# Optimization experiments

Hardware: AMD Instinct MI355X
Metric: run time of the kernel (lower is better)

Reference implementation:

```python
import jax, jax.numpy as jnp
import numpy as np

B, T = 64, 2048
HID, FAST, SLOW, VOCAB = 256, 64, 256, 64
WRITE_THRESH = 0.4
NEG = -1000000000.0


def setup_inputs() -> dict:
    key = jax.random.key(0)
    ks = jax.random.split(key, 10)
    s = 0.05  # small init so gate sigmoids are not saturated
    return {
        "seq": jax.random.randint(ks[0], (B, T), 0, VOCAB),
        "emb": jax.random.normal(ks[1], (VOCAB, HID), jnp.float32),        # encoder embedding table
        "Wg": jax.random.normal(ks[2], (HID, 1), jnp.float32) * s,         # write_gate
        "bg": jnp.zeros((1,), jnp.float32),
        "Wd": jax.random.normal(ks[3], (HID, 1), jnp.float32) * s,         # demotion_net
        "bd": jnp.zeros((1,), jnp.float32),
        "Wq": jax.random.normal(ks[4], (HID, HID), jnp.float32) * s,       # read_head.q_proj
        "bq": jnp.zeros((HID,), jnp.float32),
        "Wo": jax.random.normal(ks[5], (HID, VOCAB), jnp.float32) * s,     # read_head.out
        "bo": jnp.zeros((VOCAB,), jnp.float32),
    }


def _process_sequence(h, Wg, bg, Wd, bd):
    # h: (B, T, H). Sequential LRU tiered-memory scatter, vectorized over batch.
    Bb, Tt, H = h.shape

    def step(state, tok_h):
        fm, sm, fa, sa, fu, su = state
        ws = jax.nn.sigmoid(tok_h @ Wg + bg)[:, 0]          # (B,) write score
        act = ws >= WRITE_THRESH                            # skip rows with score < 0.4
        fa = fa + fu.astype(jnp.int32)                      # age occupied slots
        sa = sa + su.astype(jnp.int32)
        free = ~fu
        has_free = jnp.any(free, axis=1)                    # (B,)
        free_idx = jnp.argmax(free, axis=1)                 # first free fast slot
        dem = ((fm @ Wd)[..., 0] + bd[0])                   # (B, FAST) demotion scores
        dem_slot = jnp.argmin(dem, axis=1)
        fslot = jnp.where(has_free, free_idx, dem_slot)     # fast slot to write
        foh = jax.nn.one_hot(fslot, FAST, dtype=bool)
        wf = act[:, None] & foh                              # (B, FAST) fast-write mask
        # value demoted to slow (only used when fast was full)
        demoted = jnp.take_along_axis(fm, fslot[:, None, None], axis=1)[:, 0, :]
        slow_act = act & ~has_free
        sfree = ~su
        s_has_free = jnp.any(sfree, axis=1)
        ss = jnp.where(s_has_free, jnp.argmax(sfree, axis=1), jnp.argmax(sa, axis=1))
        soh = jax.nn.one_hot(ss, SLOW, dtype=bool)
        wsm = slow_act[:, None] & soh                        # (B, SLOW) slow-write mask
        sm = jnp.where(wsm[..., None], demoted[:, None, :], sm)
        sa = jnp.where(wsm, 0, sa)
        su = su | wsm
        tok = jax.lax.stop_gradient(tok_h)                   # original writes tok_h.detach()
        fm = jnp.where(wf[..., None], tok[:, None, :], fm)
        fa = jnp.where(wf, 0, fa)
        fu = fu | wf
        return (fm, sm, fa, sa, fu, su), None

    init = (
        jnp.zeros((Bb, FAST, H), h.dtype),
        jnp.zeros((Bb, SLOW, H), h.dtype),
        jnp.zeros((Bb, FAST), jnp.int32),
        jnp.zeros((Bb, SLOW), jnp.int32),
        jnp.zeros((Bb, FAST), bool),
        jnp.zeros((Bb, SLOW), bool),
    )
    hs = jnp.swapaxes(h[:, : Tt - 3], 0, 1)                  # loop runs for T-3 tokens
    (fm, sm, fa, sa, fu, su), _ = jax.lax.scan(step, init, hs)
    memory = jnp.concatenate([fm, sm], axis=1)               # (B, F+S, H)
    mask = jnp.concatenate([fu, su], axis=1).astype(h.dtype)
    slow_mask = su.astype(h.dtype)
    return memory, mask, slow_mask


def reference(seq, emb, Wg, bg, Wd, bd, Wq, bq, Wo, bo):
    h = emb[seq]                                             # encoder: (B, T, H)
    memory, mask, slow_mask = _process_sequence(h, Wg, bg, Wd, bd)
    # ReadHead
    q = h[:, -1, :] @ Wq + bq                                # (B, H)
    scores = jnp.einsum("bnh,bh->bn", memory, q)
    scores = jnp.where(mask == 0, NEG, scores)
    attn = jax.nn.softmax(scores, axis=-1)
    ctx = jnp.einsum("bn,bnh->bh", attn, memory)
    logits = ctx @ Wo + bo                                   # (B, VOCAB)
    return logits, slow_mask
```

## Files before the change

kernel.cpp:

```cpp
#include <hip/hip_runtime.h>
#include <math.h>

#define BB 64
#define TT 2048
#define HIDD 256
#define FASTN 64
#define SLOWN 256
#define VOC 64
#define TLOOP (TT - 3)
#define NEGC -1000000000.0f
#define EPAD 257
#define NEGBIG (-(1 << 20))
#define BYTEAT(U, J) ((int)(((U) >> (8 * (J))) & 0xFFu))
#define NW 16
#define NT (NW * 64)

__global__ __launch_bounds__(NT) void k_one(
    const int* __restrict__ seq, const float* __restrict__ emb,
    const float* __restrict__ Wg, const float* __restrict__ bg,
    const float* __restrict__ Wd, const float* __restrict__ bd,
    const float* __restrict__ Wq, const float* __restrict__ bq,
    const float* __restrict__ Wo, const float* __restrict__ bo,
    float* __restrict__ out) {
  const int b = blockIdx.x;
  const int tid = threadIdx.x;
  const int lane = tid & 63;
  const int wv = tid >> 6;

  __shared__ float embS[VOC * EPAD];
  __shared__ __align__(16) unsigned char zsB[2080];
  __shared__ float qLastS[HIDD], ctxS[HIDD];
  __shared__ float pp16[NW][64];
  __shared__ float gp16[NW][64], dp16[NW][64];
  __shared__ float qp4[4][HIDD];
  __shared__ float demS[64], wS[64];
  __shared__ int prS[64], invS[64], cntTok[64];
  __shared__ int CS[NW];
  __shared__ int PsS[NW][64], QsS[NW][64], eSS[NW][64];

  const int2 sq = ((const int2*)(seq + b * TT))[tid];
  const int lastv = seq[b * TT + TT - 1];
  const float4* emb4 = (const float4*)emb;
  for (int i = tid; i < VOC * 64; i += NT) {
    float4 e = emb4[i];
    float* d = &embS[(i >> 6) * EPAD + ((i & 63) << 2)];
    d[0] = e.x; d[1] = e.y; d[2] = e.z; d[3] = e.w;
  }
  __syncthreads();

  {
    const int v = tid & 63, kp = tid >> 6;
    const float* er = &embS[v * EPAD + kp * 16];
    const float* wg = &Wg[kp * 16];
    const float* wd = &Wd[kp * 16];
    float g = 0.f, d = 0.f;
#pragma unroll
    for (int k = 0; k < 16; ++k) { float e = er[k]; g += e * wg[k]; d += e * wd[k]; }
    gp16[kp][v] = g; dp16[kp][v] = d;
  }
  __syncthreads();
  if (tid < 64) {
    float g = bg[0], d = bd[0];
#pragma unroll
    for (int p = 0; p < NW; ++p) { g += gp16[p][tid]; d += dp16[p][tid]; }
    int act = (1.f / (1.f + expf(-g)) >= 0.4f) ? 1 : 0;
    demS[tid] = d;
    float dv = d;
    int r = 0;
    for (int u2 = 0; u2 < 64; ++u2) {
      float du = demS[u2];
      r += (du < dv || (du == dv && u2 < tid)) ? 1 : 0;
    }
    invS[r] = tid;
    prS[tid] = act ? r : 0xFF;
  }
  __syncthreads();

  const int t0 = tid * 2;
  int by0, by1, c;
  {
    int r0 = prS[sq.x], r1 = prS[sq.y];
    by0 = (t0 < TLOOP) ? r0 : 0xFF;
    by1 = (t0 + 1 < TLOOP) ? r1 : 0xFF;
    c = ((by0 != 0xFF) ? 1 : 0) + ((by1 != 0xFF) ? 1 : 0);
  }
  int incl = c;
  for (int s = 1; s < 64; s <<= 1) {
    int t = __shfl_up(incl, s);
    if (lane >= s) incl += t;
  }
  if (lane == 63) CS[wv] = incl;
  __syncthreads();

  int Ow = 0, A = 0;
#pragma unroll
  for (int w2 = 0; w2 < NW; ++w2) {
    int cw = CS[w2];
    Ow += (w2 < wv) ? cw : 0;
    A += cw;
  }
  {
    int pos = Ow + incl - c;
    if (by0 != 0xFF) zsB[pos++] = (unsigned char)by0;
    if (by1 != 0xFF) zsB[pos++] = (unsigned char)by1;
  }
  __syncthreads();

  const int fsplit = A < 64 ? A : 64;
  const int nL = A - fsplit;
  const int win = nL < 256 ? nL : 256;
  const int wstart = A - win;
  const int L = (((A + NW - 1) / NW) + 15) & ~15;
  const int baseW = wv * L;
  const int endW = min(baseW + L, A);

  if (tid < 256)
    out[BB * VOC + b * SLOWN + tid] = (tid < win) ? 1.0f : 0.0f;

  const int jq = tid & 255, kq = tid >> 8, kb = kq * 64;
  float wqA[32];
#pragma unroll
  for (int k = 0; k < 32; ++k) wqA[k] = Wq[(kb + k) * HIDD + jq];

  int P = 0, Q = NEGBIG;
  for (int g = baseW; g < endW; g += 16) {
    uint4 t4 = *(const uint4*)(zsB + g);
    unsigned dsw[4] = {t4.x, t4.y, t4.z, t4.w};
    const int gHi = min(g + 16, endW);
    if (gHi == g + 16 && gHi <= fsplit) {
#pragma unroll
      for (int d = 0; d < 4; ++d)
#pragma unroll
        for (int j = 0; j < 4; ++j) {
          int x = (BYTEAT(dsw[d], j) <= lane) ? 1 : 0;
          P += x; Q += x;
        }
    } else if (gHi == g + 16 && g >= fsplit) {
#pragma unroll
      for (int d = 0; d < 4; ++d)
#pragma unroll
        for (int j = 0; j < 4; ++j) {
          int x = (BYTEAT(dsw[d], j) <= lane) ? 1 : 0;
          P += x - 1;
          Q = max(Q + x - 1, x);
        }
    } else {
#pragma unroll
      for (int d = 0; d < 4; ++d)
#pragma unroll
        for (int j = 0; j < 4; ++j) {
          int i = g + d * 4 + j;
          int x = (BYTEAT(dsw[d], j) <= lane) ? 1 : 0;
          bool vld = i < endW;
          bool fil = i < fsplit;
          int p = fil ? x : x - 1;
          int q = fil ? NEGBIG : x;
          int Pn = P + p;
          int Qn = max(Q + p, q);
          P = vld ? Pn : P;
          Q = vld ? Qn : Q;
        }
    }
  }
  PsS[wv][lane] = P;
  QsS[wv][lane] = Q;
  __syncthreads();

  float qacc = 0.f;
  {
    const float* eL = &embS[lastv * EPAD + kb];
#pragma unroll
    for (int k = 0; k < 32; ++k) qacc += eL[k] * wqA[k];
  }
  float wqB[32];
#pragma unroll
  for (int k = 0; k < 32; ++k) wqB[k] = Wq[(kb + 32 + k) * HIDD + jq];

  int e = 0;
  const bool walkW = (endW > wstart);
  if (walkW) {
    int a = 0;
    for (int w2 = 0; w2 < wv; ++w2)
      a = max(a + PsS[w2][lane], QsS[w2][lane]);
    for (int g = baseW; g < endW; g += 16) {
      uint4 t4 = *(const uint4*)(zsB + g);
      unsigned dsw[4] = {t4.x, t4.y, t4.z, t4.w};
      const int gHi = min(g + 16, endW);
      const bool full = (gHi == g + 16);
      if (full && gHi <= fsplit) {
#pragma unroll
        for (int d = 0; d < 4; ++d)
#pragma unroll
          for (int j = 0; j < 4; ++j)
            a += (BYTEAT(dsw[d], j) <= lane) ? 1 : 0;
      } else if (full && g >= fsplit && gHi <= wstart) {
#pragma unroll
        for (int d = 0; d < 4; ++d)
#pragma unroll
          for (int j = 0; j < 4; ++j) {
            int xm1 = (BYTEAT(dsw[d], j) <= lane) ? 0 : -1;
            a = max(a, 1) + xm1;
          }
      } else if (full && g >= wstart) {
#pragma unroll
        for (int d = 0; d < 4; ++d)
#pragma unroll
          for (int j = 0; j < 4; ++j) {
            int xm1 = (BYTEAT(dsw[d], j) <= lane) ? 0 : -1;
            e += (a > 0) ? 1 : 0;
            a = max(a, 1) + xm1;
          }
      } else {
#pragma unroll
        for (int d = 0; d < 4; ++d)
#pragma unroll
          for (int j = 0; j < 4; ++j) {
            int i = g + d * 4 + j;
            int x = (BYTEAT(dsw[d], j) <= lane) ? 1 : 0;
            bool vld = i < endW;
            bool fil = i < fsplit;
            bool wg = vld && (i >= wstart);
            e += (wg && a > 0) ? 1 : 0;
            int af = a + x;
            int al = max(a, 1) + (x - 1);
            int an = fil ? af : al;
            a = vld ? an : a;
          }
      }
    }
  }
  eSS[wv][lane] = e;

  {
    const float* eL = &embS[lastv * EPAD + kb + 32];
#pragma unroll
    for (int k = 0; k < 32; ++k) qacc += eL[k] * wqB[k];
  }
  qp4[kq][jq] = qacc;
  __syncthreads();

  if (tid < 64) {
    int af = 0;
#pragma unroll
    for (int w2 = 0; w2 < NW; ++w2)
      af = max(af + PsS[w2][lane], QsS[w2][lane]);
    int et = 0;
#pragma unroll
    for (int w2 = 0; w2 < NW; ++w2) et += eSS[w2][lane];
    int ap = __shfl_up(af, 1); if (lane == 0) ap = 0;
    int ep = __shfl_up(et, 1); if (lane == 0) ep = 0;
    cntTok[invS[lane]] = (af - ap) + (et - ep);
  }
  if (tid < 256)
    qLastS[tid] = qp4[0][tid] + qp4[1][tid] + qp4[2][tid] + qp4[3][tid] + bq[tid];
  __syncthreads();

  const int o = tid & 63, part = tid >> 6;
  float wor[16];
#pragma unroll
  for (int k = 0; k < 16; ++k) wor[k] = Wo[((part << 4) + k) * VOC + o];

  {
    const float* er = &embS[o * EPAD + part * 16];
    const float* qr = &qLastS[part * 16];
    float s = 0.f;
#pragma unroll
    for (int k = 0; k < 16; ++k) s += er[k] * qr[k];
    pp16[part][o] = s;
  }
  __syncthreads();
  if (tid < 64) {
    float sc = 0.f;
#pragma unroll
    for (int p = 0; p < NW; ++p) sc += pp16[p][tid];
    int cc = cntTok[tid];
    float m = (cc > 0) ? sc : NEGC;
    for (int off = 32; off; off >>= 1) m = fmaxf(m, __shfl_xor(m, off));
    float w = (cc > 0) ? (float)cc * expf(sc - m) : 0.f;
    float z = w;
    for (int off = 32; off; off >>= 1) z += __shfl_xor(z, off);
    z += (float)(FASTN + SLOWN - (fsplit + win)) * expf(NEGC - m);
    wS[tid] = w / z;
  }
  __syncthreads();

  if (tid < 256) {
    float cacc = 0.f;
#pragma unroll 16
    for (int u = 0; u < 64; ++u) cacc += wS[u] * embS[u * EPAD + tid];
    ctxS[tid] = cacc;
  }
  __syncthreads();

  {
    const float* cr = &ctxS[part * 16];
    float s = 0.f;
#pragma unroll
    for (int k = 0; k < 16; ++k) s += cr[k] * wor[k];
    pp16[part][o] = s;
  }
  __syncthreads();
  if (tid < 64) {
    float s = bo[tid];
#pragma unroll
    for (int p = 0; p < NW; ++p) s += pp16[p][tid];
    out[b * VOC + tid] = s;
  }
}

extern "C" void kernel_launch(void* const* d_in, const int* in_sizes, int n_in,
                              void* d_out, int out_size, void* d_ws, size_t ws_size,
                              hipStream_t stream) {
  const int*   seq = (const int*)d_in[0];
  const float* emb = (const float*)d_in[1];
  const float* Wg  = (const float*)d_in[2];
  const float* bg  = (const float*)d_in[3];
  const float* Wd  = (const float*)d_in[4];
  const float* bd  = (const float*)d_in[5];
  const float* Wq  = (const float*)d_in[6];
  const float* bq  = (const float*)d_in[7];
  const float* Wo  = (const float*)d_in[8];
  const float* bo  = (const float*)d_in[9];
  float* out = (float*)d_out;

  k_one<<<dim3(64), dim3(NT), 0, stream>>>(seq, emb, Wg, bg, Wd, bd,
                                           Wq, bq, Wo, bo, out);
}
```

Measured before the change: 88.56 us.

## Replace per-byte max-plus scans with closed-form SWAR popcount counts

The per-wave sequential scans over the compacted slot bytes, which computed max-plus prefix pairs (P,Q) and window hit counts one byte at a time, are replaced by closed-form expressions. These use counts gathered with SWAR byte comparisons plus popcount over 4-byte words. The buffer is zero-padded after A so word reads past the end are safe. This cuts the serial integer work in both passes, but correctness now rests on the derived identities, for example that Q depends only on the last element.

```diff
diff --git a/kernel.cpp b/kernel.cpp
--- a/kernel.cpp
+++ b/kernel.cpp
@@ -11,9 +11,22 @@
 #define NEGC -1000000000.0f
 #define EPAD 257
 #define NEGBIG (-(1 << 20))
-#define BYTEAT(U, J) ((int)(((U) >> (8 * (J))) & 0xFFu))
 #define NW 16
 #define NT (NW * 64)
+
+
+__device__ __forceinline__ int countx(const unsigned char* zs, int lo, int hi,
+                                      unsigned LL8) {
+  int cnt = 0;
+  for (int d = lo & ~3; d < hi; d += 4) {
+    unsigned U = *(const unsigned*)(zs + d);
+    unsigned m = (LL8 - U) & 0x80808080u;
+    if (d < lo) m &= 0x80808080u << ((lo - d) << 3);
+    if (d + 4 > hi) m &= 0x80808080u >> ((d + 4 - hi) << 3);
+    cnt += __popc(m);
+  }
+  return cnt;
+}
 
 __global__ __launch_bounds__(NT) void k_one(
     const int* __restrict__ seq, const float* __restrict__ emb,
@@ -104,6 +117,7 @@
     if (by0 != 0xFF) zsB[pos++] = (unsigned char)by0;
     if (by1 != 0xFF) zsB[pos++] = (unsigned char)by1;
   }
+  if (tid < 16) zsB[A + tid] = 0;
   __syncthreads();
 
   const int fsplit = A < 64 ? A : 64;
@@ -122,48 +136,21 @@
 #pragma unroll
   for (int k = 0; k < 32; ++k) wqA[k] = Wq[(kb + k) * HIDD + jq];
 
-  int P = 0, Q = NEGBIG;
-  for (int g = baseW; g < endW; g += 16) {
-    uint4 t4 = *(const uint4*)(zsB + g);
-    unsigned dsw[4] = {t4.x, t4.y, t4.z, t4.w};
-    const int gHi = min(g + 16, endW);
-    if (gHi == g + 16 && gHi <= fsplit) {
-#pragma unroll
-      for (int d = 0; d < 4; ++d)
-#pragma unroll
-        for (int j = 0; j < 4; ++j) {
-          int x = (BYTEAT(dsw[d], j) <= lane) ? 1 : 0;
-          P += x; Q += x;
-        }
-    } else if (gHi == g + 16 && g >= fsplit) {
-#pragma unroll
-      for (int d = 0; d < 4; ++d)
-#pragma unroll
-        for (int j = 0; j < 4; ++j) {
-          int x = (BYTEAT(dsw[d], j) <= lane) ? 1 : 0;
-          P += x - 1;
-          Q = max(Q + x - 1, x);
-        }
-    } else {
-#pragma unroll
-      for (int d = 0; d < 4; ++d)
-#pragma unroll
-        for (int j = 0; j < 4; ++j) {
-          int i = g + d * 4 + j;
-          int x = (BYTEAT(dsw[d], j) <= lane) ? 1 : 0;
-          bool vld = i < endW;
-          bool fil = i < fsplit;
-          int p = fil ? x : x - 1;
-          int q = fil ? NEGBIG : x;
-          int Pn = P + p;
-          int Qn = max(Q + p, q);
-          P = vld ? Pn : P;
-          Q = vld ? Qn : Q;
-        }
-    }
-  }
-  PsS[wv][lane] = P;
-  QsS[wv][lane] = Q;
+  const unsigned LL8 = (unsigned)lane * 0x01010101u | 0x80808080u;
+  const int fmin = min(endW, fsplit);
+  const int lf = max(baseW, fsplit);
+  const int wbl = max(lf, min(endW, wstart));
+  int cF = 0, cPre = 0, cWin = 0;
+  if (fmin > baseW) cF = countx(zsB, baseW, fmin, LL8);
+  if (wbl > lf) cPre = countx(zsB, lf, wbl, LL8);
+  if (endW > wbl) cWin = countx(zsB, wbl, endW, LL8);
+  const int lenL = endW - lf;
+  {
+    int P = cF + cPre + cWin - (lenL > 0 ? lenL : 0);
+    int Q = (lenL > 0) ? ((zsB[endW - 1] <= lane) ? 1 : 0) : NEGBIG;
+    PsS[wv][lane] = P;
+    QsS[wv][lane] = Q;
+  }
   __syncthreads();
 
   float qacc = 0.f;
@@ -177,57 +164,21 @@
   for (int k = 0; k < 32; ++k) wqB[k] = Wq[(kb + 32 + k) * HIDD + jq];
 
   int e = 0;
-  const bool walkW = (endW > wstart);
-  if (walkW) {
+  if (endW > wbl) {
     int a = 0;
     for (int w2 = 0; w2 < wv; ++w2)
       a = max(a + PsS[w2][lane], QsS[w2][lane]);
-    for (int g = baseW; g < endW; g += 16) {
-      uint4 t4 = *(const uint4*)(zsB + g);
-      unsigned dsw[4] = {t4.x, t4.y, t4.z, t4.w};
-      const int gHi = min(g + 16, endW);
-      const bool full = (gHi == g + 16);
-      if (full && gHi <= fsplit) {
-#pragma unroll
-        for (int d = 0; d < 4; ++d)
-#pragma unroll
-          for (int j = 0; j < 4; ++j)
-            a += (BYTEAT(dsw[d], j) <= lane) ? 1 : 0;
-      } else if (full && g >= fsplit && gHi <= wstart) {
-#pragma unroll
-        for (int d = 0; d < 4; ++d)
-#pragma unroll
-          for (int j = 0; j < 4; ++j) {
-            int xm1 = (BYTEAT(dsw[d], j) <= lane) ? 0 : -1;
-            a = max(a, 1) + xm1;
-          }
-      } else if (full && g >= wstart) {
-#pragma unroll
-        for (int d = 0; d < 4; ++d)
-#pragma unroll
-          for (int j = 0; j < 4; ++j) {
-            int xm1 = (BYTEAT(dsw[d], j) <= lane) ? 0 : -1;
-            e += (a > 0) ? 1 : 0;
-            a = max(a, 1) + xm1;
-          }
-      } else {
-#pragma unroll
-        for (int d = 0; d < 4; ++d)
-#pragma unroll
-          for (int j = 0; j < 4; ++j) {
-            int i = g + d * 4 + j;
-            int x = (BYTEAT(dsw[d], j) <= lane) ? 1 : 0;
-            bool vld = i < endW;
-            bool fil = i < fsplit;
-            bool wg = vld && (i >= wstart);
-            e += (wg && a > 0) ? 1 : 0;
-            int af = a + x;
-            int al = max(a, 1) + (x - 1);
-            int an = fil ? af : al;
-            a = vld ? an : a;
-          }
-      }
+    a += cF;
+    const int lenP = wbl - lf;
+    if (lenP > 0) {
+      int xl = (zsB[wbl - 1] <= lane) ? 1 : 0;
+      a = max(a + cPre - lenP, xl);
     }
+    const int n = endW - wbl;
+    const int xw = (zsB[endW - 1] <= lane) ? 1 : 0;
+    const int Zp = (n - cWin) - (1 - xw);
+    const int F = max(0, Zp - a + 1);
+    e = n - F;
   }
   eSS[wv][lane] = e;
 
```

After: 85.46 us. 3.5% less time.
